# Kernel tuning notes

Hardware: AMD Instinct MI355X
Metric: run time of the kernel (lower is better)

The kernel has to match this reference:

```python
import jax, jax.numpy as jnp
import numpy as np
import math

D_MODEL = 384
N_HEADS = 3
D_K = D_MODEL // N_HEADS  # 128
LN_EPS = 1e-6


def entmax15(z, axis=-1):
    """Exact 1.5-entmax (Peters et al. 2019), sort-based."""
    z = z / 2.0
    z = z - jnp.max(z, axis=axis, keepdims=True)
    zs = -jnp.sort(-z, axis=axis)                      # descending
    K = z.shape[axis]
    rho = jnp.arange(1, K + 1, dtype=z.dtype)          # broadcasts on last axis
    mean = jnp.cumsum(zs, axis=axis) / rho
    mean_sq = jnp.cumsum(zs * zs, axis=axis) / rho
    ss = rho * (mean_sq - mean * mean)
    delta = (1.0 - ss) / rho
    tau = mean - jnp.sqrt(jnp.clip(delta, 0.0))
    support = jnp.sum(tau <= zs, axis=axis, keepdims=True)  # support size
    tau_star = jnp.take_along_axis(tau, support - 1, axis=axis)
    p = jnp.clip(z - tau_star, 0.0)
    return p * p


def layer_norm(x, a, b):
    # matches torch module: std with Bessel correction (unbiased), eps added to std
    mean = jnp.mean(x, axis=-1, keepdims=True)
    n = x.shape[-1]
    var = jnp.sum((x - mean) ** 2, axis=-1, keepdims=True) / (n - 1)
    std = jnp.sqrt(var)
    return a * (x - mean) / (std + LN_EPS) + b


def setup_inputs() -> dict:
    key = jax.random.key(0)
    ks = jax.random.split(key, 8)
    B, N = 2, 2048
    scale = 1.0 / math.sqrt(D_MODEL)
    x = jax.random.normal(ks[0], (B, D_MODEL, N), dtype=jnp.float32)
    wq = jax.random.uniform(ks[1], (D_MODEL, D_MODEL), jnp.float32, -scale, scale)
    bq = jax.random.uniform(ks[2], (D_MODEL,), jnp.float32, -scale, scale)
    wk = jax.random.uniform(ks[3], (D_MODEL, D_MODEL), jnp.float32, -scale, scale)
    bk = jax.random.uniform(ks[4], (D_MODEL,), jnp.float32, -scale, scale)
    wv = jax.random.uniform(ks[5], (D_MODEL, D_MODEL), jnp.float32, -scale, scale)
    bv = jax.random.uniform(ks[6], (D_MODEL,), jnp.float32, -scale, scale)
    ln_a = jnp.ones((D_MODEL,), jnp.float32)
    ln_b = jnp.ones((D_MODEL,), jnp.float32)
    return {"x": x, "wq": wq, "bq": bq, "wk": wk, "bk": bk,
            "wv": wv, "bv": bv, "ln_a": ln_a, "ln_b": ln_b}


def reference(x, wq, bq, wk, bk, wv, bv, ln_a, ln_b):
    B = x.shape[0]
    xt = jnp.transpose(x, (0, 2, 1))                   # [B, N, C]
    x1 = xt

    def proj(w, b):
        y = jnp.einsum('bnc,oc->bno', xt, w) + b       # [B, N, C]
        return jnp.transpose(y.reshape(B, -1, N_HEADS, D_K), (0, 2, 1, 3))

    q = proj(wq, bq)                                   # [B, h, N, d_k]
    k = proj(wk, bk)
    v = proj(wv, bv)

    energy = jnp.einsum('bhqd,bhkd->bhqk', q, k) / math.sqrt(D_K)
    attn = entmax15(energy, axis=-1)                   # sparse attention weights
    out = jnp.einsum('bhqk,bhkd->bhqd', attn, v)       # [B, h, N, d_k]
    out = jnp.transpose(out, (0, 2, 1, 3)).reshape(B, -1, N_HEADS * D_K)
    # dropout layers are identity in eval mode
    return x1 + layer_norm(out, ln_a, ln_b)
```

## Files before the change

### kernel.cpp

```cpp
#include <hip/hip_runtime.h>
#include <hip/hip_fp16.h>
#include <math.h>

#define DM   384
#define NH   3
#define DK   128
#define NSEQ 2048
#define BATCH 2
#define NTOK (BATCH*NSEQ)
#define SEG  (BATCH*NSEQ*DM)
#define NEWTON_IT 6
#define QT   16
#define ZP   520

typedef __attribute__((ext_vector_type(8))) short     bf16x8;
typedef __attribute__((ext_vector_type(4))) float     f32x4;
typedef __attribute__((ext_vector_type(8))) _Float16  h8;
typedef __attribute__((ext_vector_type(4))) _Float16  h4;
typedef __attribute__((ext_vector_type(2))) _Float16  h2v;

#if __has_builtin(__builtin_amdgcn_fdot2)
#define HAVE_FDOT2 1
#else
#define HAVE_FDOT2 0
#endif

__device__ __forceinline__ unsigned short f2bf(float f) {
  unsigned u = __builtin_bit_cast(unsigned, f);
  u += 0x7FFFu + ((u >> 16) & 1u);
  return (unsigned short)(u >> 16);
}

__global__ __launch_bounds__(256) void transpose_k(const float* __restrict__ x,
                                                   float* __restrict__ xT,
                                                   unsigned short* __restrict__ xbf) {
  __shared__ float tile[32][33];
  int b  = blockIdx.z;
  int cB = blockIdx.y * 32;
  int nB = blockIdx.x * 32;
  int tx = threadIdx.x & 31, ty = threadIdx.x >> 5;
#pragma unroll
  for (int i = 0; i < 4; i++)
    tile[ty + i*8][tx] = x[((size_t)b*DM + cB + ty + i*8)*NSEQ + nB + tx];
  __syncthreads();
#pragma unroll
  for (int i = 0; i < 4; i++) {
    float v = tile[tx][ty + i*8];
    size_t row = (size_t)b*NSEQ + nB + ty + i*8;
    xT [row*DM + cB + tx] = v;
    xbf[row*DM + cB + tx] = f2bf(v);
  }
}

__global__ __launch_bounds__(256) void wconv_k(const float* __restrict__ wq,
    const float* __restrict__ wk, const float* __restrict__ wv,
    unsigned short* __restrict__ wbf) {
  int pj = blockIdx.y;
  const float* src = (pj == 0) ? wq : (pj == 1) ? wk : wv;
  int i = (blockIdx.x * 256 + threadIdx.x) * 4;
  float4 v = *(const float4*)(src + i);
  ushort4 o;
  o.x = f2bf(v.x); o.y = f2bf(v.y); o.z = f2bf(v.z); o.w = f2bf(v.w);
  *(ushort4*)(wbf + (size_t)pj*DM*DM + i) = o;
}

__global__ __launch_bounds__(256) void proj_mfma_k(
    const unsigned short* __restrict__ xbf,
    const unsigned short* __restrict__ wbf,
    const float* __restrict__ bq, const float* __restrict__ bk, const float* __restrict__ bv,
    unsigned short* __restrict__ Qo, unsigned short* __restrict__ Ko,
    unsigned short* __restrict__ VTo) {
  int tid = threadIdx.x, lane = tid & 63, w = tid >> 6;
  int g = lane >> 4, li = lane & 15;
  int wr = w >> 1, wc = w & 1;
  int h  = blockIdx.y;
  int pj = blockIdx.z;
  const unsigned short* wp0 = wbf + (size_t)pj * DM * DM;
  const float* bias = (pj == 0) ? bq : (pj == 1) ? bk : bv;

  const unsigned short *Am, *Bn;
  int mB, nB;
  if (pj < 2) { Am = wp0; mB = h*128 + wr*64;          Bn = xbf; nB = blockIdx.x*128 + wc*64; }
  else        { Am = xbf; mB = blockIdx.x*128 + wr*64; Bn = wp0; nB = h*128 + wc*64; }

  f32x4 acc[4][4];
#pragma unroll
  for (int fi = 0; fi < 4; fi++)
#pragma unroll
    for (int fj = 0; fj < 4; fj++) acc[fi][fj] = (f32x4){0.f, 0.f, 0.f, 0.f};

#pragma unroll 2
  for (int ks = 0; ks < DM/32; ks++) {
    bf16x8 af[4], bf[4];
#pragma unroll
    for (int fi = 0; fi < 4; fi++)
      af[fi] = *(const bf16x8*)(Am + (size_t)(mB + fi*16 + li)*DM + ks*32 + g*8);
#pragma unroll
    for (int fj = 0; fj < 4; fj++)
      bf[fj] = *(const bf16x8*)(Bn + (size_t)(nB + fj*16 + li)*DM + ks*32 + g*8);
#pragma unroll
    for (int fi = 0; fi < 4; fi++)
#pragma unroll
      for (int fj = 0; fj < 4; fj++)
        acc[fi][fj] = __builtin_amdgcn_mfma_f32_16x16x32_bf16(af[fi], bf[fj], acc[fi][fj], 0, 0, 0);
  }

  if (pj < 2) {
    unsigned short* dst = (pj == 0) ? Qo : Ko;
#pragma unroll
    for (int fi = 0; fi < 4; fi++) {
      int o0 = mB + fi*16 + g*4;
      float4 bb = *(const float4*)(bias + o0);
      int d0 = o0 & 127;
#pragma unroll
      for (int fj = 0; fj < 4; fj++) {
        int tok = nB + fj*16 + li;
        int bb_ = tok >> 11, n = tok & 2047;
        ushort4 v4;
        v4.x = f2bf(acc[fi][fj][0] + bb.x);
        v4.y = f2bf(acc[fi][fj][1] + bb.y);
        v4.z = f2bf(acc[fi][fj][2] + bb.z);
        v4.w = f2bf(acc[fi][fj][3] + bb.w);
        *(ushort4*)(dst + ((size_t)(bb_*NH + h)*NSEQ + n)*DK + d0) = v4;
      }
    }
  } else {
#pragma unroll
    for (int fj = 0; fj < 4; fj++) {
      int o  = nB + fj*16 + li;
      float bb = bias[o];
      int d  = o & 127;
#pragma unroll
      for (int fi = 0; fi < 4; fi++) {
        int tok0 = mB + fi*16 + g*4;
        int bb_ = tok0 >> 11, n0 = tok0 & 2047;
        ushort4 v4;
        v4.x = __builtin_bit_cast(unsigned short, (_Float16)(acc[fi][fj][0] + bb));
        v4.y = __builtin_bit_cast(unsigned short, (_Float16)(acc[fi][fj][1] + bb));
        v4.z = __builtin_bit_cast(unsigned short, (_Float16)(acc[fi][fj][2] + bb));
        v4.w = __builtin_bit_cast(unsigned short, (_Float16)(acc[fi][fj][3] + bb));
        *(ushort4*)(VTo + ((size_t)(bb_*NH + h)*DK + d)*NSEQ + n0) = v4;
      }
    }
  }
}

__device__ __forceinline__ void scan16(const h2v* zh, float tau,
                                       float& f, float& g, float& c) {
  float ff = 0.f, gg = 0.f, cc = 0.f;
#if HAVE_FDOT2
  _Float16 th = (_Float16)tau;
  h2v t2 = {th, th};
  h2v zero2 = {(_Float16)0.f, (_Float16)0.f};
  h2v one2  = {(_Float16)1.f, (_Float16)1.f};
  h2v big2  = {(_Float16)60000.f, (_Float16)60000.f};
#pragma unroll
  for (int i = 0; i < 16; i++) {
    h2v d = __builtin_elementwise_max(zh[i] - t2, zero2);
    ff = __builtin_amdgcn_fdot2(d, d, ff, false);
    gg = __builtin_amdgcn_fdot2(d, one2, gg, false);
    h2v mm = __builtin_elementwise_min(d * big2, one2);
    cc = __builtin_amdgcn_fdot2(mm, one2, cc, false);
  }
#else
#pragma unroll
  for (int i = 0; i < 16; i++) {
#pragma unroll
    for (int j = 0; j < 2; j++) {
      float z = (float)zh[i][j];
      float d = fmaxf(z - tau, 0.f);
      ff = fmaf(d, d, ff);
      gg += d;
      cc += (d > 0.f) ? 1.f : 0.f;
    }
  }
#endif
  f = ff; g = gg; c = cc;
}

__device__ __forceinline__ float nstep(float tau, float f, float g, float c, float m) {
  float num  = f - 1.0f;
  float disc = fmaxf(g*g - c*num, 0.f);
  float den  = (num >= 0.f) ? (g + sqrtf(disc)) : (2.0f * g);
  float t = tau + num / fmaxf(den, 1e-12f);
  return fminf(t, m - 0.01f);
}

__global__ __launch_bounds__(256, 3) void attn_k(const unsigned short* __restrict__ Qb,
    const unsigned short* __restrict__ Kb, const _Float16* __restrict__ VTb,
    float* __restrict__ AO) {
  __shared__ _Float16 zc[2][QT * ZP];

  int tid = threadIdx.x, lane = tid & 63, w = tid >> 6;
  int g = lane >> 4, li = lane & 15;
  int swz = (blockIdx.x & 7) * 96 + (blockIdx.x >> 3);
  int bh = swz / (NSEQ/QT), qb = swz % (NSEQ/QT);
  int qbase = qb * QT;
  const unsigned short* Qh  = Qb  + (size_t)bh * NSEQ * DK;
  const unsigned short* Kh  = Kb  + (size_t)bh * NSEQ * DK;
  const _Float16*       VTh = VTb + (size_t)bh * DK * NSEQ;
  const float zs = 0.044194173824159216f;

  bf16x8 bq[4];
#pragma unroll
  for (int ks = 0; ks < 4; ks++)
    bq[ks] = *(const bf16x8*)(Qh + (size_t)(qbase + li)*DK + ks*32 + g*8);

  h8 zr[4][4];
#pragma unroll
  for (int c = 0; c < 4; c++) {
    _Float16* buf = zc[c & 1];
#pragma unroll
    for (int kt = 0; kt < 8; kt++) {
      int krow = c*512 + w*128 + kt*16 + li;
      bf16x8 bk[4];
#pragma unroll
      for (int ks = 0; ks < 4; ks++)
        bk[ks] = *(const bf16x8*)(Kh + (size_t)krow*DK + ks*32 + g*8);
      f32x4 za = (f32x4){0.f,0.f,0.f,0.f};
#pragma unroll
      for (int ks = 0; ks < 4; ks++)
        za = __builtin_amdgcn_mfma_f32_16x16x32_bf16(bk[ks], bq[ks], za, 0, 0, 0);
      h4 p;
#pragma unroll
      for (int r = 0; r < 4; r++) p[r] = (_Float16)(za[r] * zs);
      *(h4*)(buf + (size_t)li*ZP + w*128 + kt*16 + g*4) = p;
    }
    __syncthreads();
#pragma unroll
    for (int r = 0; r < 4; r++)
      zr[r][c] = *(const h8*)(buf + (size_t)(w*4 + r)*ZP + lane*8);
  }

  float tau[4], mx[4];
#pragma unroll
  for (int r = 0; r < 4; r++) {
    union { h8 v[4]; h2v h[16]; } u;
#pragma unroll
    for (int c = 0; c < 4; c++) u.v[c] = zr[r][c];
    h2v m2 = u.h[0];
#pragma unroll
    for (int i = 1; i < 16; i++) m2 = __builtin_elementwise_max(m2, u.h[i]);
    float m = fmaxf((float)m2[0], (float)m2[1]);
#pragma unroll
    for (int off = 32; off > 0; off >>= 1) m = fmaxf(m, __shfl_xor(m, off));
    mx[r] = m;
    tau[r] = m - 1.0f;
  }
  for (int it = 0; it < NEWTON_IT; ++it) {
    float f[4], gg[4], cc[4];
#pragma unroll
    for (int r = 0; r < 4; r++) {
      union { h8 v[4]; h2v h[16]; } ur;
#pragma unroll
      for (int c = 0; c < 4; c++) ur.v[c] = zr[r][c];
      scan16(ur.h, tau[r], f[r], gg[r], cc[r]);
    }
#pragma unroll
    for (int off = 32; off > 0; off >>= 1) {
#pragma unroll
      for (int r = 0; r < 4; r++) {
        f[r]  += __shfl_xor(f[r],  off);
        gg[r] += __shfl_xor(gg[r], off);
        cc[r] += __shfl_xor(cc[r], off);
      }
    }
#pragma unroll
    for (int r = 0; r < 4; r++) tau[r] = nstep(tau[r], f[r], gg[r], cc[r], mx[r]);
  }

  int d0 = w * 32;
  f32x4 pacc[2];
  pacc[0] = (f32x4){0.f,0.f,0.f,0.f};
  pacc[1] = (f32x4){0.f,0.f,0.f,0.f};
#pragma unroll
  for (int c = 0; c < 4; c++) {
    _Float16* buf = zc[c & 1];
#pragma unroll
    for (int r = 0; r < 4; r++) {
      union { h8 v; h2v h[4]; } u;
      u.v = zr[r][c];
      _Float16 th = (_Float16)tau[r];
      h2v t2 = {th, th};
      h2v zero2 = {(_Float16)0.f, (_Float16)0.f};
#pragma unroll
      for (int j = 0; j < 4; j++) {
        h2v d = __builtin_elementwise_max(u.h[j] - t2, zero2);
        u.h[j] = d * d;
      }
      *(h8*)(buf + (size_t)(w*4 + r)*ZP + lane*8) = u.v;
    }
    __syncthreads();
#pragma unroll
    for (int kk = 0; kk < 16; kk++) {
      h8 pa  = *(const h8*)(buf + (size_t)li*ZP + kk*32 + g*8);
      h8 bv0 = *(const h8*)(VTh + (size_t)(d0 + li)*NSEQ + c*512 + kk*32 + g*8);
      h8 bv1 = *(const h8*)(VTh + (size_t)(d0 + 16 + li)*NSEQ + c*512 + kk*32 + g*8);
      pacc[0] = __builtin_amdgcn_mfma_f32_16x16x32_f16(pa, bv0, pacc[0], 0, 0, 0);
      pacc[1] = __builtin_amdgcn_mfma_f32_16x16x32_f16(pa, bv1, pacc[1], 0, 0, 0);
    }
  }

  int b = bh / NH, h = bh % NH;
#pragma unroll
  for (int dt = 0; dt < 2; dt++)
#pragma unroll
    for (int r = 0; r < 4; r++)
      AO[((size_t)b*NSEQ + qbase + g*4 + r)*DM + h*DK + d0 + dt*16 + li] = pacc[dt][r];
}

__global__ __launch_bounds__(256) void ln_k(const float* __restrict__ AO,
    const float* __restrict__ xT, const float* __restrict__ ga,
    const float* __restrict__ gb, float* __restrict__ outp) {
  int lane = threadIdx.x & 63;
  int wave = threadIdx.x >> 6;
  int row  = blockIdx.x * 4 + wave;
  const float* ao = AO + (size_t)row*DM;
  float2 c0 = *(const float2*)(ao + lane*2);
  float2 c1 = *(const float2*)(ao + 128 + lane*2);
  float2 c2 = *(const float2*)(ao + 256 + lane*2);
  float s  = c0.x + c0.y + c1.x + c1.y + c2.x + c2.y;
  float ss = c0.x*c0.x + c0.y*c0.y + c1.x*c1.x + c1.y*c1.y + c2.x*c2.x + c2.y*c2.y;
#pragma unroll
  for (int off = 32; off > 0; off >>= 1) {
    s  += __shfl_xor(s,  off);
    ss += __shfl_xor(ss, off);
  }
  float mean = s * (1.0f / 384.0f);
  float var  = (ss - 384.0f*mean*mean) * (1.0f / 383.0f);
  var = fmaxf(var, 0.f);
  float inv = 1.0f / (sqrtf(var) + 1e-6f);
  const float* xr = xT + (size_t)row*DM;
  float* op = outp + (size_t)row*DM;
#pragma unroll
  for (int ch = 0; ch < 3; ch++) {
    int i0 = ch*128 + lane*2;
    float2 g  = *(const float2*)(ga + i0);
    float2 bb = *(const float2*)(gb + i0);
    float2 xv = *(const float2*)(xr + i0);
    float2 av = (ch == 0) ? c0 : (ch == 1) ? c1 : c2;
    float2 o;
    o.x = g.x*(av.x - mean)*inv + bb.x + xv.x;
    o.y = g.y*(av.y - mean)*inv + bb.y + xv.y;
    *(float2*)(op + i0) = o;
  }
}

extern "C" void kernel_launch(void* const* d_in, const int* in_sizes, int n_in,
                              void* d_out, int out_size, void* d_ws, size_t ws_size,
                              hipStream_t stream) {
  const float* x  = (const float*)d_in[0];
  const float* wq = (const float*)d_in[1];
  const float* bq = (const float*)d_in[2];
  const float* wk = (const float*)d_in[3];
  const float* bk = (const float*)d_in[4];
  const float* wv = (const float*)d_in[5];
  const float* bv = (const float*)d_in[6];
  const float* la = (const float*)d_in[7];
  const float* lb = (const float*)d_in[8];
  float* out = (float*)d_out;

  char* wsb = (char*)d_ws;
  float* xT = (float*)wsb;
  float* AO = (float*)(wsb + (size_t)SEG*4);
  unsigned short* Qb  = (unsigned short*)(wsb + (size_t)SEG*8);
  unsigned short* Kb  = (unsigned short*)(wsb + (size_t)SEG*8 + (size_t)SEG*2);
  unsigned short* VT  = (unsigned short*)(wsb + (size_t)SEG*8 + (size_t)SEG*4);
  unsigned short* xbf = (unsigned short*)(wsb + (size_t)SEG*8 + (size_t)SEG*6);
  unsigned short* wbf = (unsigned short*)(wsb + (size_t)SEG*8 + (size_t)SEG*8);

  hipLaunchKernelGGL(transpose_k, dim3(NSEQ/32, DM/32, BATCH), dim3(256), 0, stream,
                     x, xT, xbf);
  hipLaunchKernelGGL(wconv_k, dim3(DM*DM/1024, 3), dim3(256), 0, stream, wq, wk, wv, wbf);
  hipLaunchKernelGGL(proj_mfma_k, dim3(NTOK/128, NH, 3), dim3(256), 0, stream,
                     xbf, wbf, bq, bk, bv, Qb, Kb, VT);
  hipLaunchKernelGGL(attn_k, dim3(BATCH*NH*(NSEQ/QT)), dim3(256), 0, stream,
                     Qb, Kb, (const _Float16*)VT, AO);
  hipLaunchKernelGGL(ln_k, dim3(BATCH*NSEQ/4), dim3(256), 0, stream, AO, xT, la, lb, out);
}
```

Before: 134.5 us.

## Stage K and V tiles through swizzled LDS with async global_load_lds double-buffering

Instead of each wave reading K and V^T straight from global memory into registers, the attention kernel now copies 64-key tiles of K and V into a double-buffered LDS staging area with global_load_lds. The staging uses an XOR swizzle, and the MFMA operands are then read from LDS. The goal is to overlap the next tile's load with the current tile's MFMAs and to make the global accesses more coalesced and better reused. In exchange it adds a __syncthreads per 64-key step and more LDS use (about 33 KB per block), which could hurt occupancy at 3 blocks per CU.

```diff
diff --git a/kernel.cpp b/kernel.cpp
--- a/kernel.cpp
+++ b/kernel.cpp
@@ -24,6 +24,12 @@
 #else
 #define HAVE_FDOT2 0
 #endif
+
+typedef const unsigned int __attribute__((address_space(1)))* gas1_t;
+typedef unsigned int __attribute__((address_space(3)))* las3_t;
+__device__ __forceinline__ void gll16(const void* g, void* l) {
+  __builtin_amdgcn_global_load_lds((gas1_t)g, (las3_t)l, 16, 0, 0);
+}
 
 __device__ __forceinline__ unsigned short f2bf(float f) {
   unsigned u = __builtin_bit_cast(unsigned, f);
@@ -189,7 +195,8 @@
 __global__ __launch_bounds__(256, 3) void attn_k(const unsigned short* __restrict__ Qb,
     const unsigned short* __restrict__ Kb, const _Float16* __restrict__ VTb,
     float* __restrict__ AO) {
-  __shared__ _Float16 zc[2][QT * ZP];
+  __shared__ _Float16 stg[2][8192];
+  __shared__ _Float16 zbuf[QT * ZP];
 
   int tid = threadIdx.x, lane = tid & 63, w = tid >> 6;
   int g = lane >> 4, li = lane & 15;
@@ -206,17 +213,44 @@
   for (int ks = 0; ks < 4; ks++)
     bq[ks] = *(const bf16x8*)(Qh + (size_t)(qbase + li)*DK + ks*32 + g*8);
 
+  auto stageK = [&](int c, int s, int b) {
+#pragma unroll
+    for (int j = 0; j < 4; j++) {
+      int idx   = (j*4 + w)*64 + lane;
+      int row_l = idx >> 4;
+      int ch    = idx & 15;
+      const unsigned short* src = Kh + (size_t)(c*512 + s*64 + row_l)*DK
+                                     + ((ch ^ (row_l & 7)) * 8);
+      void* dst = (void*)((char*)&stg[b][0] + (size_t)(j*4 + w) * 1024);
+      gll16(src, dst);
+    }
+  };
+  auto stageV = [&](int c, int s, int b) {
+#pragma unroll
+    for (int j = 0; j < 4; j++) {
+      int idx = (j*4 + w)*64 + lane;
+      int dr  = idx >> 3;
+      int ch  = idx & 7;
+      const _Float16* src = VTh + (size_t)dr*NSEQ + c*512 + s*64
+                                + ((ch ^ (dr & 7)) * 8);
+      void* dst = (void*)((char*)&stg[b][0] + (size_t)(j*4 + w) * 1024);
+      gll16(src, dst);
+    }
+  };
+
   h8 zr[4][4];
 #pragma unroll
   for (int c = 0; c < 4; c++) {
-    _Float16* buf = zc[c & 1];
-#pragma unroll
-    for (int kt = 0; kt < 8; kt++) {
-      int krow = c*512 + w*128 + kt*16 + li;
+    stageK(c, 0, 0);
+    __syncthreads();
+    for (int s = 0; s < 8; s++) {
+      if (s < 7) stageK(c, s + 1, (s + 1) & 1);
+      const _Float16* kb = &stg[s & 1][0];
       bf16x8 bk[4];
 #pragma unroll
       for (int ks = 0; ks < 4; ks++)
-        bk[ks] = *(const bf16x8*)(Kh + (size_t)krow*DK + ks*32 + g*8);
+        bk[ks] = *(const bf16x8*)(kb + (size_t)(w*16 + li)*128
+                                     + (((ks*4 + g) ^ (li & 7)) * 8));
       f32x4 za = (f32x4){0.f,0.f,0.f,0.f};
 #pragma unroll
       for (int ks = 0; ks < 4; ks++)
@@ -224,12 +258,13 @@
       h4 p;
 #pragma unroll
       for (int r = 0; r < 4; r++) p[r] = (_Float16)(za[r] * zs);
-      *(h4*)(buf + (size_t)li*ZP + w*128 + kt*16 + g*4) = p;
-    }
+      *(h4*)(zbuf + (size_t)li*ZP + s*64 + w*16 + g*4) = p;
+      __syncthreads();
+    }
+#pragma unroll
+    for (int r = 0; r < 4; r++)
+      zr[r][c] = *(const h8*)(zbuf + (size_t)(w*4 + r)*ZP + lane*8);
     __syncthreads();
-#pragma unroll
-    for (int r = 0; r < 4; r++)
-      zr[r][c] = *(const h8*)(buf + (size_t)(w*4 + r)*ZP + lane*8);
   }
 
   float tau[4], mx[4];
@@ -269,13 +304,11 @@
     for (int r = 0; r < 4; r++) tau[r] = nstep(tau[r], f[r], gg[r], cc[r], mx[r]);
   }
 
-  int d0 = w * 32;
   f32x4 pacc[2];
   pacc[0] = (f32x4){0.f,0.f,0.f,0.f};
   pacc[1] = (f32x4){0.f,0.f,0.f,0.f};
 #pragma unroll
   for (int c = 0; c < 4; c++) {
-    _Float16* buf = zc[c & 1];
 #pragma unroll
     for (int r = 0; r < 4; r++) {
       union { h8 v; h2v h[4]; } u;
@@ -288,16 +321,24 @@
         h2v d = __builtin_elementwise_max(u.h[j] - t2, zero2);
         u.h[j] = d * d;
       }
-      *(h8*)(buf + (size_t)(w*4 + r)*ZP + lane*8) = u.v;
-    }
+      *(h8*)(zbuf + (size_t)(w*4 + r)*ZP + lane*8) = u.v;
+    }
+    stageV(c, 0, 0);
     __syncthreads();
-#pragma unroll
-    for (int kk = 0; kk < 16; kk++) {
-      h8 pa  = *(const h8*)(buf + (size_t)li*ZP + kk*32 + g*8);
-      h8 bv0 = *(const h8*)(VTh + (size_t)(d0 + li)*NSEQ + c*512 + kk*32 + g*8);
-      h8 bv1 = *(const h8*)(VTh + (size_t)(d0 + 16 + li)*NSEQ + c*512 + kk*32 + g*8);
-      pacc[0] = __builtin_amdgcn_mfma_f32_16x16x32_f16(pa, bv0, pacc[0], 0, 0, 0);
-      pacc[1] = __builtin_amdgcn_mfma_f32_16x16x32_f16(pa, bv1, pacc[1], 0, 0, 0);
+    for (int s = 0; s < 8; s++) {
+      if (s < 7) stageV(c, s + 1, (s + 1) & 1);
+      const _Float16* vb = &stg[s & 1][0];
+#pragma unroll
+      for (int k2 = 0; k2 < 2; k2++) {
+        h8 pa = *(const h8*)(zbuf + (size_t)li*ZP + s*64 + k2*32 + g*8);
+#pragma unroll
+        for (int dt = 0; dt < 2; dt++) {
+          int dr = w*32 + dt*16 + li;
+          h8 bv = *(const h8*)(vb + (size_t)dr*64 + (((k2*4 + g) ^ (dr & 7)) * 8));
+          pacc[dt] = __builtin_amdgcn_mfma_f32_16x16x32_f16(pa, bv, pacc[dt], 0, 0, 0);
+        }
+      }
+      __syncthreads();
     }
   }
 
@@ -306,7 +347,7 @@
   for (int dt = 0; dt < 2; dt++)
 #pragma unroll
     for (int r = 0; r < 4; r++)
-      AO[((size_t)b*NSEQ + qbase + g*4 + r)*DM + h*DK + d0 + dt*16 + li] = pacc[dt][r];
+      AO[((size_t)b*NSEQ + qbase + g*4 + r)*DM + h*DK + w*32 + dt*16 + li] = pacc[dt][r];
 }
 
 __global__ __launch_bounds__(256) void ln_k(const float* __restrict__ AO,
```

Result: faster. 118.6 us (-11.8%).
